# Kernel optimization log

Measured on AMD Instinct MI355X. Metric: run time of the kernel, lower is better.

Reference implementation:

```python
import jax, jax.numpy as jnp
import numpy as np

BIG = 1e6  # sentinel larger than any image coordinate


def _edt_sq(mask):
    """Exact squared Euclidean distance transform of a 2D bool mask.

    Returns, for every pixel, the squared distance to the nearest True pixel.
    Separable algorithm: exact 1D EDT along axis 0 (two cummax scans), then a
    brute-force-but-vectorized lower-envelope min along axis 1.
    """
    H, W = mask.shape

    def nearest_below(m):
        # distance (along axis 0) to nearest True at index <= i, per column
        idx = jnp.arange(H, dtype=jnp.float32)[:, None]
        pos = jnp.where(m, idx, -BIG)
        return idx - jax.lax.cummax(pos, axis=0)

    d_down = nearest_below(mask)
    d_up = nearest_below(mask[::-1])[::-1]
    d1 = jnp.minimum(jnp.minimum(d_down, d_up), BIG)  # [H, W] axis-0 distance
    f = d1 * d1  # squared

    j = jnp.arange(W, dtype=jnp.float32)
    offs = (j[:, None] - j[None, :]) ** 2  # [W_out, W_k]
    # D[i,j] = min_k ( (j-k)^2 + f[i,k] )   -> [H, W, W] intermediate
    return jnp.min(f[:, None, :] + offs[None, :, :], axis=-1)


def _hausdorff_one(a, b):
    """Symmetric Hausdorff distance between bool masks a, b ([H, W]).
    NaN if either mask is empty (matches scipy/monai behaviour handled by loss)."""
    dt_b = jnp.sqrt(_edt_sq(b))  # distance of every pixel to set b
    dt_a = jnp.sqrt(_edt_sq(a))
    h_ab = jnp.max(jnp.where(a, dt_b, 0.0))  # max_{x in a} d(x, b)
    h_ba = jnp.max(jnp.where(b, dt_a, 0.0))
    hd = jnp.maximum(h_ab, h_ba)
    empty = jnp.logical_or(~jnp.any(a), ~jnp.any(b))
    return jnp.where(empty, jnp.nan, hd)


def setup_inputs() -> dict:
    key = jax.random.key(0)
    k1, k2 = jax.random.split(key)
    inputs = jax.random.uniform(k1, (8, 512, 512), dtype=jnp.float32)
    targets = jax.random.uniform(k2, (8, 512, 512), dtype=jnp.float32)
    return {"inputs": inputs, "targets": targets}


def reference(inputs, targets):
    a = inputs > 0.5
    b = targets > 0.5
    # sequential over batch to bound the [H, W, W] EDT intermediate
    hds = jax.lax.map(lambda ab: _hausdorff_one(ab[0], ab[1]), (a, b))
    # NaN (empty mask) -> 1, else 1 - 1/(1 + hd)
    to_mean = jnp.where(jnp.isnan(hds), 1.0, 1.0 - 1.0 / (1.0 + hds))
    return jnp.mean(to_mean)
```

## Files before the change

kernel.cpp:

```cpp
#include <hip/hip_runtime.h>
#include <hip/hip_bf16.h>

static constexpr int H = 512;
static constexpr int W = 512;
static constexpr int NIMG = 8;


__device__ __forceinline__ int edt_d(unsigned int m, int r, int row0, int ig,
                                     int carry_dn, int carry_up) {
    unsigned int below = m & (0xFFFFFFFFu >> (31 - r));
    int pos_dn = below ? (row0 + (31 - __clz((int)below))) : carry_dn;
    unsigned int above = m & (0xFFFFFFFFu << r);
    int pos_up = above ? (row0 + (__ffs((int)above) - 1)) : carry_up;
    return min(ig - pos_dn, pos_up - ig);
}

__global__ __launch_bounds__(512)
void k_col_edt(const float* __restrict__ A, const float* __restrict__ B,
               unsigned short* __restrict__ F, unsigned int* __restrict__ bm,
               float* __restrict__ maxsq, int* __restrict__ anyflag,
               int* __restrict__ done, int* __restrict__ gdone) {
    const int tid  = threadIdx.x;
    const int quad = tid & 7;
    const int seg  = tid >> 3;
    const int sub  = seg & 3;
    const int win  = seg >> 2;
    const int cg   = blockIdx.x;
    const int m16  = blockIdx.y;

    if (cg == 0 && m16 == 0) {
        if (tid < 16)       { maxsq[tid] = 0.0f; anyflag[tid] = 0; }
        else if (tid < 32)  { done[(tid - 16) * 32] = 0; }
        else if (tid == 32) { *gdone = 0; }
    }

    const int colbase = cg * 32 + quad * 4;
    const float* src = (m16 < NIMG) ? (A + (size_t)m16 * H * W)
                                    : (B + (size_t)(m16 - NIMG) * H * W);
    unsigned short* f = F + (size_t)m16 * H * W;
    const int row0 = seg * 8;
    const int w0   = win * 32;

    unsigned int m0 = 0, m1 = 0, m2 = 0, m3 = 0;
    #pragma unroll
    for (int r = 0; r < 8; ++r) {
        float4 v = *reinterpret_cast<const float4*>(src + (size_t)(row0 + r) * W + colbase);
        m0 |= (v.x > 0.5f ? 1u : 0u) << r;
        m1 |= (v.y > 0.5f ? 1u : 0u) << r;
        m2 |= (v.z > 0.5f ? 1u : 0u) << r;
        m3 |= (v.w > 0.5f ? 1u : 0u) << r;
    }

    const int sh = 8 * sub;
    m0 <<= sh; m1 <<= sh; m2 <<= sh; m3 <<= sh;
    m0 |= __shfl_xor(m0, 8, 64);  m0 |= __shfl_xor(m0, 16, 64);
    m1 |= __shfl_xor(m1, 8, 64);  m1 |= __shfl_xor(m1, 16, 64);
    m2 |= __shfl_xor(m2, 8, 64);  m2 |= __shfl_xor(m2, 16, 64);
    m3 |= __shfl_xor(m3, 8, 64);  m3 |= __shfl_xor(m3, 16, 64);

    const int NEGS = -(1 << 21), POSS = (1 << 21);
    __shared__ int s_hi[16][32];
    __shared__ int s_lo[16][32];
    if (sub == 0) {
        int4 hi, lo;
        hi.x = m0 ? (w0 + 31 - __clz((int)m0)) : NEGS;
        hi.y = m1 ? (w0 + 31 - __clz((int)m1)) : NEGS;
        hi.z = m2 ? (w0 + 31 - __clz((int)m2)) : NEGS;
        hi.w = m3 ? (w0 + 31 - __clz((int)m3)) : NEGS;
        lo.x = m0 ? (w0 + __ffs((int)m0) - 1) : POSS;
        lo.y = m1 ? (w0 + __ffs((int)m1) - 1) : POSS;
        lo.z = m2 ? (w0 + __ffs((int)m2) - 1) : POSS;
        lo.w = m3 ? (w0 + __ffs((int)m3) - 1) : POSS;
        *reinterpret_cast<int4*>(&s_hi[win][quad * 4]) = hi;
        *reinterpret_cast<int4*>(&s_lo[win][quad * 4]) = lo;
        uint4 o = make_uint4(m0, m1, m2, m3);
        *reinterpret_cast<uint4*>(&bm[((size_t)m16 * 16 + win) * W + colbase]) = o;
    }
    __syncthreads();

    int4 cdn = {NEGS, NEGS, NEGS, NEGS};
    for (int t = 0; t < win; ++t) {
        int4 h = *reinterpret_cast<int4*>(&s_hi[t][quad * 4]);
        cdn.x = max(cdn.x, h.x); cdn.y = max(cdn.y, h.y);
        cdn.z = max(cdn.z, h.z); cdn.w = max(cdn.w, h.w);
    }
    int4 cup = {POSS, POSS, POSS, POSS};
    for (int t = win + 1; t < 16; ++t) {
        int4 l = *reinterpret_cast<int4*>(&s_lo[t][quad * 4]);
        cup.x = min(cup.x, l.x); cup.y = min(cup.y, l.y);
        cup.z = min(cup.z, l.z); cup.w = min(cup.w, l.w);
    }

    #pragma unroll
    for (int k = 0; k < 8; ++k) {
        const int ig = row0 + k;
        const int rb = sh + k;
        ushort4 o;
        o.x = (unsigned short)min(edt_d(m0, rb, w0, ig, cdn.x, cup.x), 65535);
        o.y = (unsigned short)min(edt_d(m1, rb, w0, ig, cdn.y, cup.y), 65535);
        o.z = (unsigned short)min(edt_d(m2, rb, w0, ig, cdn.z, cup.z), 65535);
        o.w = (unsigned short)min(edt_d(m3, rb, w0, ig, cdn.w, cup.w), 65535);
        *reinterpret_cast<ushort4*>(f + (size_t)ig * W + colbase) = o;
    }
}

__global__ __launch_bounds__(512)
void k_row_env(const unsigned short* __restrict__ F, const unsigned int* __restrict__ bm,
               float* __restrict__ maxsq, int* __restrict__ anyflag,
               int* __restrict__ done, int* __restrict__ gdone,
               float* __restrict__ out) {
    const int task = blockIdx.y;
    const int rg   = blockIdx.x;
    const int img  = task & 7;
    const int dir  = task >> 3;
    const int wave = threadIdx.x >> 6;
    const int lane = threadIdx.x & 63;
    const int fsel = (dir == 0) ? (NIMG + img) : img;
    const int msel = (dir == 0) ? img : (NIMG + img);
    const int p0 = lane * 8;

    __shared__ float sf[8][512];
    __shared__ float s_wmax[8];
    __shared__ int   s_wany[8];

    const unsigned int* brow = bm + ((size_t)msel * 16 + rg) * W + p0;
    uint4 b0 = *reinterpret_cast<const uint4*>(brow);
    uint4 b1 = *reinterpret_cast<const uint4*>(brow + 4);

    float vmax = 0.0f;
    int   vany = 0;

    #pragma unroll 1
    for (int it = 0; it < 4; ++it) {
        const int row = rg * 32 + it * 8 + wave;
        const unsigned short* frow = F + (size_t)fsel * H * W + (size_t)row * W;
        uint4 fu = *reinterpret_cast<const uint4*>(frow + p0);
        const int bit = it * 8 + wave;

        float w[24];
        {
            unsigned int uu[4] = {fu.x, fu.y, fu.z, fu.w};
            #pragma unroll
            for (int e = 0; e < 4; ++e) {
                int dl = (int)(uu[e] & 0xFFFFu);
                int dh = (int)(uu[e] >> 16);
                w[8 + 2 * e]     = (dl == 65535) ? 1.0e12f : (float)(dl * dl);
                w[8 + 2 * e + 1] = (dh == 65535) ? 1.0e12f : (float)(dh * dh);
            }
        }
        #pragma unroll
        for (int e = 0; e < 8; ++e) {
            w[e]      = __shfl_up(w[8 + e], 1, 64);
            w[16 + e] = __shfl_down(w[8 + e], 1, 64);
        }
        if (lane == 0) {
            #pragma unroll
            for (int e = 0; e < 8; ++e) w[e] = 1.0e12f;
        }
        if (lane == 63) {
            #pragma unroll
            for (int e = 0; e < 8; ++e) w[16 + e] = 1.0e12f;
        }

        bool mk[8];
        mk[0] = (b0.x >> bit) & 1u; mk[1] = (b0.y >> bit) & 1u;
        mk[2] = (b0.z >> bit) & 1u; mk[3] = (b0.w >> bit) & 1u;
        mk[4] = (b1.x >> bit) & 1u; mk[5] = (b1.y >> bit) & 1u;
        mk[6] = (b1.z >> bit) & 1u; mk[7] = (b1.w >> bit) & 1u;
        #pragma unroll
        for (int p = 0; p < 8; ++p) vany |= (int)mk[p];

        float best[8];
        #pragma unroll
        for (int p = 0; p < 8; ++p) best[p] = w[8 + p];
        #pragma unroll
        for (int r = 1; r <= 8; ++r) {
            const float rr = (float)(r * r);
            #pragma unroll
            for (int p = 0; p < 8; ++p)
                best[p] = fminf(best[p], fminf(rr + w[8 + p - r], rr + w[8 + p + r]));
        }

        float bmax = 0.0f;
        #pragma unroll
        for (int p = 0; p < 8; ++p) bmax = fmaxf(bmax, mk[p] ? best[p] : 0.0f);
        if (!__all(bmax <= 81.0f)) {
            float* srow = &sf[wave][0];
            *reinterpret_cast<float4*>(srow + p0)     = make_float4(w[8],  w[9],  w[10], w[11]);
            *reinterpret_cast<float4*>(srow + p0 + 4) = make_float4(w[12], w[13], w[14], w[15]);
            for (int r = 9; r < W; ++r) {
                const float rr = (float)(r * r);
                if (__all(rr >= bmax)) break;
                #pragma unroll
                for (int p = 0; p < 8; ++p) {
                    int kl = p0 + p - r, kr = p0 + p + r;
                    float cl = (kl >= 0) ? srow[kl] : 1.0e12f;
                    float cr = (kr < W)  ? srow[kr] : 1.0e12f;
                    best[p] = fminf(best[p], fminf(rr + cl, rr + cr));
                }
                bmax = 0.0f;
                #pragma unroll
                for (int p = 0; p < 8; ++p) bmax = fmaxf(bmax, mk[p] ? best[p] : 0.0f);
            }
        }

        #pragma unroll
        for (int p = 0; p < 8; ++p) vmax = fmaxf(vmax, mk[p] ? best[p] : 0.0f);
    }

    #pragma unroll
    for (int off = 32; off > 0; off >>= 1)
        vmax = fmaxf(vmax, __shfl_down(vmax, off, 64));
    int wany = __any(vany) ? 1 : 0;
    if (lane == 0) { s_wmax[wave] = vmax; s_wany[wave] = wany; }
    __syncthreads();
    if (threadIdx.x == 0) {
        float mx = s_wmax[0]; int af = s_wany[0];
        #pragma unroll
        for (int q = 1; q < 8; ++q) { mx = fmaxf(mx, s_wmax[q]); af |= s_wany[q]; }
        atomicMax((int*)&maxsq[task], __float_as_int(mx));
        if (af) atomicOr(&anyflag[msel], 1);
        asm volatile("s_waitcnt vmcnt(0)" ::: "memory");
        int p = atomicAdd(&done[task * 32], 1);
        if (p == (int)gridDim.x - 1) {
            int g = atomicAdd(gdone, 1);
            if (g == 15) {
                float s = 0.0f;
                for (int i2 = 0; i2 < NIMG; ++i2) {
                    int af1 = __hip_atomic_load(&anyflag[i2],        __ATOMIC_RELAXED, __HIP_MEMORY_SCOPE_AGENT);
                    int af2 = __hip_atomic_load(&anyflag[NIMG + i2], __ATOMIC_RELAXED, __HIP_MEMORY_SCOPE_AGENT);
                    float m1 = __hip_atomic_load(&maxsq[i2],         __ATOMIC_RELAXED, __HIP_MEMORY_SCOPE_AGENT);
                    float m2 = __hip_atomic_load(&maxsq[NIMG + i2],  __ATOMIC_RELAXED, __HIP_MEMORY_SCOPE_AGENT);
                    float loss;
                    if (!af1 || !af2) {
                        loss = 1.0f;
                    } else {
                        float hd = sqrtf(fmaxf(m1, m2));
                        loss = 1.0f - 1.0f / (1.0f + hd);
                    }
                    s += loss;
                }
                out[0] = s * (1.0f / (float)NIMG);
            }
        }
    }
}

extern "C" void kernel_launch(void* const* d_in, const int* in_sizes, int n_in,
                              void* d_out, int out_size, void* d_ws, size_t ws_size,
                              hipStream_t stream) {
    const float* A = (const float*)d_in[0];
    const float* B = (const float*)d_in[1];
    char* base = (char*)d_ws;
    unsigned short* F = (unsigned short*)base;
    char* meta        = base + (size_t)16 * H * W * sizeof(unsigned short);
    float* maxsq      = (float*)(meta + 0);
    int*   anyflag    = (int*)(meta + 64);
    int*   done       = (int*)(meta + 256);
    int*   gdone      = (int*)(meta + 2304);
    unsigned int* bm  = (unsigned int*)(meta + 4096);
    float* out        = (float*)d_out;

    hipLaunchKernelGGL(k_col_edt, dim3(W / 32, 16), dim3(512), 0, stream,
                       A, B, F, bm, maxsq, anyflag, done, gdone);
    hipLaunchKernelGGL(k_row_env, dim3(16, 16), dim3(512), 0, stream,
                       F, bm, maxsq, anyflag, done, gdone, out);
}
```

Before: 25.85 us.

## Recompute column EDT in row kernel from bitmasks instead of storing F

The first kernel no longer writes the full 16x512x512 ushort column-distance array. It stores only per-window carry positions (nearest set row above and below each 32-row window), packed as int16 pairs. The second kernel rebuilds each column distance on the fly from the bitmask and these carries. This removes about 8 MB of global writes and reads in exchange for a few extra bit operations per element. Sentinels are reduced to ±20000 so they fit in 16 bits, which changes the squared value for empty columns from 1e12 to roughly (2e4)^2.

```diff
diff --git a/kernel.cpp b/kernel.cpp
--- a/kernel.cpp
+++ b/kernel.cpp
@@ -6,18 +6,12 @@
 static constexpr int NIMG = 8;
 
 
-__device__ __forceinline__ int edt_d(unsigned int m, int r, int row0, int ig,
-                                     int carry_dn, int carry_up) {
-    unsigned int below = m & (0xFFFFFFFFu >> (31 - r));
-    int pos_dn = below ? (row0 + (31 - __clz((int)below))) : carry_dn;
-    unsigned int above = m & (0xFFFFFFFFu << r);
-    int pos_up = above ? (row0 + (__ffs((int)above) - 1)) : carry_up;
-    return min(ig - pos_dn, pos_up - ig);
-}
+static constexpr int NEGS = -20000;
+static constexpr int POSS =  20000;
 
 __global__ __launch_bounds__(512)
 void k_col_edt(const float* __restrict__ A, const float* __restrict__ B,
-               unsigned short* __restrict__ F, unsigned int* __restrict__ bm,
+               unsigned int* __restrict__ bm, unsigned int* __restrict__ cc,
                float* __restrict__ maxsq, int* __restrict__ anyflag,
                int* __restrict__ done, int* __restrict__ gdone) {
     const int tid  = threadIdx.x;
@@ -37,7 +31,6 @@
     const int colbase = cg * 32 + quad * 4;
     const float* src = (m16 < NIMG) ? (A + (size_t)m16 * H * W)
                                     : (B + (size_t)(m16 - NIMG) * H * W);
-    unsigned short* f = F + (size_t)m16 * H * W;
     const int row0 = seg * 8;
     const int w0   = win * 32;
 
@@ -58,7 +51,6 @@
     m2 |= __shfl_xor(m2, 8, 64);  m2 |= __shfl_xor(m2, 16, 64);
     m3 |= __shfl_xor(m3, 8, 64);  m3 |= __shfl_xor(m3, 16, 64);
 
-    const int NEGS = -(1 << 21), POSS = (1 << 21);
     __shared__ int s_hi[16][32];
     __shared__ int s_lo[16][32];
     if (sub == 0) {
@@ -78,34 +70,30 @@
     }
     __syncthreads();
 
-    int4 cdn = {NEGS, NEGS, NEGS, NEGS};
-    for (int t = 0; t < win; ++t) {
-        int4 h = *reinterpret_cast<int4*>(&s_hi[t][quad * 4]);
-        cdn.x = max(cdn.x, h.x); cdn.y = max(cdn.y, h.y);
-        cdn.z = max(cdn.z, h.z); cdn.w = max(cdn.w, h.w);
-    }
-    int4 cup = {POSS, POSS, POSS, POSS};
-    for (int t = win + 1; t < 16; ++t) {
-        int4 l = *reinterpret_cast<int4*>(&s_lo[t][quad * 4]);
-        cup.x = min(cup.x, l.x); cup.y = min(cup.y, l.y);
-        cup.z = min(cup.z, l.z); cup.w = min(cup.w, l.w);
-    }
-
-    #pragma unroll
-    for (int k = 0; k < 8; ++k) {
-        const int ig = row0 + k;
-        const int rb = sh + k;
-        ushort4 o;
-        o.x = (unsigned short)min(edt_d(m0, rb, w0, ig, cdn.x, cup.x), 65535);
-        o.y = (unsigned short)min(edt_d(m1, rb, w0, ig, cdn.y, cup.y), 65535);
-        o.z = (unsigned short)min(edt_d(m2, rb, w0, ig, cdn.z, cup.z), 65535);
-        o.w = (unsigned short)min(edt_d(m3, rb, w0, ig, cdn.w, cup.w), 65535);
-        *reinterpret_cast<ushort4*>(f + (size_t)ig * W + colbase) = o;
+    if (sub == 0) {
+        int4 cdn = {NEGS, NEGS, NEGS, NEGS};
+        for (int t = 0; t < win; ++t) {
+            int4 h = *reinterpret_cast<int4*>(&s_hi[t][quad * 4]);
+            cdn.x = max(cdn.x, h.x); cdn.y = max(cdn.y, h.y);
+            cdn.z = max(cdn.z, h.z); cdn.w = max(cdn.w, h.w);
+        }
+        int4 cup = {POSS, POSS, POSS, POSS};
+        for (int t = win + 1; t < 16; ++t) {
+            int4 l = *reinterpret_cast<int4*>(&s_lo[t][quad * 4]);
+            cup.x = min(cup.x, l.x); cup.y = min(cup.y, l.y);
+            cup.z = min(cup.z, l.z); cup.w = min(cup.w, l.w);
+        }
+        uint4 pk;
+        pk.x = ((unsigned)cdn.x & 0xFFFFu) | ((unsigned)cup.x << 16);
+        pk.y = ((unsigned)cdn.y & 0xFFFFu) | ((unsigned)cup.y << 16);
+        pk.z = ((unsigned)cdn.z & 0xFFFFu) | ((unsigned)cup.z << 16);
+        pk.w = ((unsigned)cdn.w & 0xFFFFu) | ((unsigned)cup.w << 16);
+        *reinterpret_cast<uint4*>(&cc[((size_t)m16 * 16 + win) * W + colbase]) = pk;
     }
 }
 
 __global__ __launch_bounds__(512)
-void k_row_env(const unsigned short* __restrict__ F, const unsigned int* __restrict__ bm,
+void k_row_env(const unsigned int* __restrict__ bm, const unsigned int* __restrict__ cc,
                float* __restrict__ maxsq, int* __restrict__ anyflag,
                int* __restrict__ done, int* __restrict__ gdone,
                float* __restrict__ out) {
@@ -118,6 +106,7 @@
     const int fsel = (dir == 0) ? (NIMG + img) : img;
     const int msel = (dir == 0) ? img : (NIMG + img);
     const int p0 = lane * 8;
+    const int w0 = rg * 32;
 
     __shared__ float sf[8][512];
     __shared__ float s_wmax[8];
@@ -126,28 +115,44 @@
     const unsigned int* brow = bm + ((size_t)msel * 16 + rg) * W + p0;
     uint4 b0 = *reinterpret_cast<const uint4*>(brow);
     uint4 b1 = *reinterpret_cast<const uint4*>(brow + 4);
+    const unsigned int* erow = bm + ((size_t)fsel * 16 + rg) * W + p0;
+    uint4 e0 = *reinterpret_cast<const uint4*>(erow);
+    uint4 e1 = *reinterpret_cast<const uint4*>(erow + 4);
+    const unsigned int* crow = cc + ((size_t)fsel * 16 + rg) * W + p0;
+    uint4 c0 = *reinterpret_cast<const uint4*>(crow);
+    uint4 c1 = *reinterpret_cast<const uint4*>(crow + 4);
+
+    unsigned int mw[8] = {e0.x, e0.y, e0.z, e0.w, e1.x, e1.y, e1.z, e1.w};
+    unsigned int mb[8] = {b0.x, b0.y, b0.z, b0.w, b1.x, b1.y, b1.z, b1.w};
+    int cd[8], cu[8];
+    {
+        unsigned int cwv[8] = {c0.x, c0.y, c0.z, c0.w, c1.x, c1.y, c1.z, c1.w};
+        #pragma unroll
+        for (int e = 0; e < 8; ++e) {
+            cd[e] = (int)(short)(cwv[e] & 0xFFFFu);
+            cu[e] = (int)(short)(cwv[e] >> 16);
+        }
+    }
 
     float vmax = 0.0f;
     int   vany = 0;
 
     #pragma unroll 1
     for (int it = 0; it < 4; ++it) {
-        const int row = rg * 32 + it * 8 + wave;
-        const unsigned short* frow = F + (size_t)fsel * H * W + (size_t)row * W;
-        uint4 fu = *reinterpret_cast<const uint4*>(frow + p0);
         const int bit = it * 8 + wave;
+        const int row = w0 + bit;
 
         float w[24];
-        {
-            unsigned int uu[4] = {fu.x, fu.y, fu.z, fu.w};
-            #pragma unroll
-            for (int e = 0; e < 4; ++e) {
-                int dl = (int)(uu[e] & 0xFFFFu);
-                int dh = (int)(uu[e] >> 16);
-                w[8 + 2 * e]     = (dl == 65535) ? 1.0e12f : (float)(dl * dl);
-                w[8 + 2 * e + 1] = (dh == 65535) ? 1.0e12f : (float)(dh * dh);
-            }
-        }
+        #pragma unroll
+        for (int e = 0; e < 8; ++e) {
+            unsigned int below = mw[e] & (0xFFFFFFFFu >> (31 - bit));
+            int pos_dn = below ? (w0 + 31 - __clz((int)below)) : cd[e];
+            unsigned int above = mw[e] & (0xFFFFFFFFu << bit);
+            int pos_up = above ? (w0 + __ffs((int)above) - 1) : cu[e];
+            int d = min(row - pos_dn, pos_up - row);
+            w[8 + e] = (float)(d * d);
+        }
+
         #pragma unroll
         for (int e = 0; e < 8; ++e) {
             w[e]      = __shfl_up(w[8 + e], 1, 64);
@@ -163,10 +168,8 @@
         }
 
         bool mk[8];
-        mk[0] = (b0.x >> bit) & 1u; mk[1] = (b0.y >> bit) & 1u;
-        mk[2] = (b0.z >> bit) & 1u; mk[3] = (b0.w >> bit) & 1u;
-        mk[4] = (b1.x >> bit) & 1u; mk[5] = (b1.y >> bit) & 1u;
-        mk[6] = (b1.z >> bit) & 1u; mk[7] = (b1.w >> bit) & 1u;
+        #pragma unroll
+        for (int e = 0; e < 8; ++e) mk[e] = (mb[e] >> bit) & 1u;
         #pragma unroll
         for (int p = 0; p < 8; ++p) vany |= (int)mk[p];
 
@@ -252,17 +255,16 @@
     const float* A = (const float*)d_in[0];
     const float* B = (const float*)d_in[1];
     char* base = (char*)d_ws;
-    unsigned short* F = (unsigned short*)base;
-    char* meta        = base + (size_t)16 * H * W * sizeof(unsigned short);
-    float* maxsq      = (float*)(meta + 0);
-    int*   anyflag    = (int*)(meta + 64);
-    int*   done       = (int*)(meta + 256);
-    int*   gdone      = (int*)(meta + 2304);
-    unsigned int* bm  = (unsigned int*)(meta + 4096);
+    float* maxsq      = (float*)(base + 0);
+    int*   anyflag    = (int*)(base + 64);
+    int*   done       = (int*)(base + 256);
+    int*   gdone      = (int*)(base + 2304);
+    unsigned int* bm  = (unsigned int*)(base + 4096);
+    unsigned int* cc  = (unsigned int*)(base + 4096 + 512 * 1024);
     float* out        = (float*)d_out;
 
     hipLaunchKernelGGL(k_col_edt, dim3(W / 32, 16), dim3(512), 0, stream,
-                       A, B, F, bm, maxsq, anyflag, done, gdone);
+                       A, B, bm, cc, maxsq, anyflag, done, gdone);
     hipLaunchKernelGGL(k_row_env, dim3(16, 16), dim3(512), 0, stream,
-                       F, bm, maxsq, anyflag, done, gdone, out);
+                       bm, cc, maxsq, anyflag, done, gdone, out);
 }
```

After: 22.04 us, median of 2. 14.8% less time.
